# Kernel optimization log

Hardware: AMD Instinct MI355X
Metric: run time of the kernel (lower is better)

Reference implementation:

```python
import jax, jax.numpy as jnp
import numpy as np

B, CIN, COUT = 4, 512, 64
T, H, W = 16, 32, 32


def conv1x1(x, w, b=None):
    # 1x1x1 Conv3d == per-voxel linear: w (out, in), x (b, in, t, h, w)
    y = jnp.einsum('oc,bcthw->bothw', w, x)
    if b is not None:
        y = y + b[None, :, None, None, None]
    return y


def setup_inputs() -> dict:
    key = jax.random.key(0)
    ks = jax.random.split(key, 9)
    def kaiming(k, fan_out_shape):
        out_c, in_c = fan_out_shape
        std = np.sqrt(2.0 / out_c)  # fan_out mode for 1x1x1 kernel
        return jax.random.normal(k, fan_out_shape, dtype=jnp.float32) * std
    c4, c8 = CIN // 4, CIN // 8
    return {
        'x': jax.random.normal(ks[0], (B, CIN, T, H, W), dtype=jnp.float32),
        'w_add1': kaiming(ks[1], (CIN, CIN)), 'b_add1': jnp.zeros((CIN,), jnp.float32),
        'w_add2': kaiming(ks[2], (CIN, CIN)), 'b_add2': jnp.zeros((CIN,), jnp.float32),
        'w_occ1': kaiming(ks[3], (c4, CIN)), 'b_occ1': jnp.zeros((c4,), jnp.float32),
        'w_occ2': kaiming(ks[4], (c8, c4)), 'b_occ2': jnp.zeros((c8,), jnp.float32),
        'w_occ3': kaiming(ks[5], (COUT, c8)),  # bias=False
    }


def reference(x, w_add1, b_add1, w_add2, b_add2, w_occ1, b_occ1, w_occ2, b_occ2, w_occ3):
    # feature_map = add_on_layer(x): conv -> relu -> conv
    feat = conv1x1(jax.nn.relu(conv1x1(x, w_add1, b_add1)), w_add2, b_add2)
    # occ_map = abs(occ(x)): conv -> relu -> conv -> relu -> conv(no bias)
    h = jax.nn.relu(conv1x1(x, w_occ1, b_occ1))
    h = jax.nn.relu(conv1x1(h, w_occ2, b_occ2))
    occ = jnp.abs(conv1x1(h, w_occ3))  # (B, COUT, T, H, W)
    # output with pool='avg': mean over spatial of occ[:, :, None] * feat[:, None]
    # == einsum contraction over T*H*W, avoiding the (B,COUT,CIN,T,H,W) intermediate
    S = T * H * W
    out = jnp.einsum('bothw,bcthw->boc', occ, feat) / S  # (B, COUT, CIN)
    return out
```

## Files before the change

kernel.cpp:

```cpp
#include <hip/hip_runtime.h>


#define S_TOT 16384

typedef __attribute__((ext_vector_type(8))) short bf8_t;
typedef __attribute__((ext_vector_type(4))) short s4_t;
typedef __attribute__((ext_vector_type(4))) float f4_t;

#define MFMA __builtin_amdgcn_mfma_f32_16x16x32_bf16

__device__ __forceinline__ short f2bf(float f) {
  union { float f; unsigned u; } v; v.f = f;
  unsigned u = v.u + 0x7FFFu + ((v.u >> 16) & 1u);
  return (short)(u >> 16);
}

__device__ __forceinline__ void glds16(const void* g, void* l) {
  __builtin_amdgcn_global_load_lds(
      (const __attribute__((address_space(1))) void*)g,
      (__attribute__((address_space(3))) void*)l, 16, 0, 0);
}

__device__ __forceinline__ void stage16k(const short* g, short* lds,
                                         int wv, int lane) {
#pragma unroll
  for (int i = 0; i < 4; ++i) {
    const int off = (wv * 4 + i) * 512;
    glds16(g + off + lane * 8, lds + off);
  }
}

__global__ __launch_bounds__(256) void k_convert(
    const float* __restrict__ w1, const float* __restrict__ wo1,
    const float* __restrict__ wo2, const float* __restrict__ wo3,
    short* __restrict__ dst) {
  int i = blockIdx.x * 256 + threadIdx.x;
  if (i < 262144) {
    const int j = i >> 9, k = i & 511;
    const int di = ((j >> 7) * 8 + (k >> 6)) * 8192 + ((k >> 3) & 7) * 1024 +
                   (j & 127) * 8 + (k & 7);
    dst[di] = f2bf(w1[i]);
  } else if (i < 327680) {
    const int e = i - 262144;
    const int c4 = e >> 9, k = e & 511;
    const int di = 262144 + (k >> 6) * 8192 + ((k >> 3) & 7) * 1024 +
                   c4 * 8 + (k & 7);
    dst[di] = f2bf(wo1[e]);
  } else if (i < 335872) {
    dst[i] = f2bf(wo2[i - 327680]);
  } else if (i < 339968) {
    dst[i] = f2bf(wo3[i - 335872]);
  }
}

__global__ __launch_bounds__(256) void k_transpose(
    const float* __restrict__ x, short* __restrict__ xTs) {
  __shared__ float tls[64][65];
  const int sb = blockIdx.x, cb = blockIdx.y, b = blockIdx.z;
  const int t = threadIdx.x;
  {
    const int cr = t >> 2, ss = (t & 3) * 16;
    const float* src = x + ((size_t)b * 512 + cb * 64 + cr) * S_TOT + sb * 64 + ss;
    f4_t v0 = *(const f4_t*)(src);
    f4_t v1 = *(const f4_t*)(src + 4);
    f4_t v2 = *(const f4_t*)(src + 8);
    f4_t v3 = *(const f4_t*)(src + 12);
#pragma unroll
    for (int j = 0; j < 4; ++j) {
      tls[cr][ss + j]      = v0[j];
      tls[cr][ss + 4 + j]  = v1[j];
      tls[cr][ss + 8 + j]  = v2[j];
      tls[cr][ss + 12 + j] = v3[j];
    }
  }
  __syncthreads();
  {
    const int sr = t >> 2, cs = (t & 3) * 16;
    alignas(16) short tmp[16];
#pragma unroll
    for (int j = 0; j < 16; ++j) tmp[j] = f2bf(tls[cs + j][sr]);
    const int st = sb >> 1, s_in = (sb & 1) * 64 + sr, k8 = cs >> 3;
    short* base = xTs + (((size_t)(b * 128 + st) * 8 + cb) * 8 + k8) * 1024 +
                  s_in * 8;
    *(bf8_t*)base          = *(const bf8_t*)&tmp[0];
    *(bf8_t*)(base + 1024) = *(const bf8_t*)&tmp[8];
  }
}

__global__ __launch_bounds__(256) void k_occ(
    const short* __restrict__ xTs, const short* __restrict__ wo1,
    const short* __restrict__ wo2, const short* __restrict__ wo3,
    const float* __restrict__ bo1, const float* __restrict__ bo2,
    short* __restrict__ occP, float* __restrict__ sumocc) {
  __shared__ short smem[32768];
  short* const buf0 = smem;
  short* const buf1 = smem + 16384;
  short* const h1s = buf0;
  short* const h2s = buf1;
  const int tile = blockIdx.x, b = blockIdx.y;
  const int t = threadIdx.x, lane = t & 63, wv = t >> 6;
  const int q = lane >> 4, li = lane & 15;
  const int mh = (wv & 1) * 64, nh = (wv >> 1) * 64;
  const short* xTb = xTs + (size_t)(b * 128 + tile) * 65536;
  const f4_t fz = {0.f, 0.f, 0.f, 0.f};

  f4_t acc[4][4];
#pragma unroll
  for (int i = 0; i < 4; ++i)
#pragma unroll
    for (int j = 0; j < 4; ++j) acc[i][j] = fz;

  stage16k(xTb, buf1, wv, lane);
  stage16k(wo1, buf1 + 8192, wv, lane);
  int cur = 1;
  for (int i = 0; i < 8; ++i) {
    __syncthreads();
    if (i < 7) {
      short* nb_ = cur ? buf0 : buf1;
      stage16k(xTb + (i + 1) * 8192, nb_, wv, lane);
      stage16k(wo1 + (i + 1) * 8192, nb_ + 8192, wv, lane);
    }
    const short* xs = cur ? buf1 : buf0;
    const short* wsp = xs + 8192;
#pragma unroll
    for (int kk = 0; kk < 2; ++kk) {
      const int pl = (4 * kk + q) * 128;
      bf8_t a[4], bb[4];
#pragma unroll
      for (int ma = 0; ma < 4; ++ma)
        a[ma] = *(const bf8_t*)&wsp[(pl + mh + 16 * ma + li) * 8];
#pragma unroll
      for (int nb = 0; nb < 4; ++nb)
        bb[nb] = *(const bf8_t*)&xs[(pl + nh + 16 * nb + li) * 8];
#pragma unroll
      for (int ma = 0; ma < 4; ++ma)
#pragma unroll
        for (int nb = 0; nb < 4; ++nb)
          acc[ma][nb] = MFMA(a[ma], bb[nb], acc[ma][nb], 0, 0, 0);
    }
    cur ^= 1;
  }
  __syncthreads();
#pragma unroll
  for (int ma = 0; ma < 4; ++ma) {
    const int c40 = mh + 16 * ma + 4 * q;
    f4_t bv = *(const f4_t*)(bo1 + c40);
#pragma unroll
    for (int nb = 0; nb < 4; ++nb) {
      const int sl = nh + 16 * nb + li;
      s4_t p;
#pragma unroll
      for (int r = 0; r < 4; ++r) p[r] = f2bf(fmaxf(acc[ma][nb][r] + bv[r], 0.0f));
      *(s4_t*)&h1s[((c40 >> 3) * 128 + sl) * 8 + (c40 & 7)] = p;
    }
  }
  __syncthreads();
  f4_t a2[4][2];
#pragma unroll
  for (int i = 0; i < 4; ++i) { a2[i][0] = fz; a2[i][1] = fz; }
#pragma unroll
  for (int kk = 0; kk < 4; ++kk) {
    const int pl = (4 * kk + q) * 128;
    bf8_t a[4], bb[2];
#pragma unroll
    for (int ma = 0; ma < 4; ++ma)
      a[ma] = *(const bf8_t*)(wo2 + (size_t)(16 * ma + li) * 128 + kk * 32 + q * 8);
#pragma unroll
    for (int nb = 0; nb < 2; ++nb)
      bb[nb] = *(const bf8_t*)&h1s[(pl + 32 * wv + 16 * nb + li) * 8];
#pragma unroll
    for (int ma = 0; ma < 4; ++ma)
#pragma unroll
      for (int nb = 0; nb < 2; ++nb)
        a2[ma][nb] = MFMA(a[ma], bb[nb], a2[ma][nb], 0, 0, 0);
  }
#pragma unroll
  for (int ma = 0; ma < 4; ++ma) {
    const int c80 = 16 * ma + 4 * q;
    f4_t bv = *(const f4_t*)(bo2 + c80);
#pragma unroll
    for (int nb = 0; nb < 2; ++nb) {
      const int sl = 32 * wv + 16 * nb + li;
      s4_t p;
#pragma unroll
      for (int r = 0; r < 4; ++r) p[r] = f2bf(fmaxf(a2[ma][nb][r] + bv[r], 0.0f));
      *(s4_t*)&h2s[((c80 >> 3) * 128 + sl) * 8 + (c80 & 7)] = p;
    }
  }
  f4_t a3[4][2];
#pragma unroll
  for (int i = 0; i < 4; ++i) { a3[i][0] = fz; a3[i][1] = fz; }
#pragma unroll
  for (int kk = 0; kk < 2; ++kk) {
    const int pl = (4 * kk + q) * 128;
    bf8_t a[4], bb[2];
#pragma unroll
    for (int ma = 0; ma < 4; ++ma)
      a[ma] = *(const bf8_t*)(wo3 + (size_t)(16 * ma + li) * 64 + kk * 32 + q * 8);
#pragma unroll
    for (int nb = 0; nb < 2; ++nb)
      bb[nb] = *(const bf8_t*)&h2s[(pl + 32 * wv + 16 * nb + li) * 8];
#pragma unroll
    for (int ma = 0; ma < 4; ++ma)
#pragma unroll
      for (int nb = 0; nb < 2; ++nb)
        a3[ma][nb] = MFMA(a[ma], bb[nb], a3[ma][nb], 0, 0, 0);
  }
  short* ot = occP + (size_t)(b * 128 + tile) * 8192;
#pragma unroll
  for (int ma = 0; ma < 4; ++ma)
#pragma unroll
    for (int nb = 0; nb < 2; ++nb) {
      const int o = 16 * ma + 4 * q;
      const int sl = 32 * wv + 16 * nb + li;
#pragma unroll
      for (int r = 0; r < 4; ++r)
        ot[(sl >> 3) * 512 + (o + r) * 8 + (sl & 7)] = f2bf(fabsf(a3[ma][nb][r]));
    }
#pragma unroll
  for (int ma = 0; ma < 4; ++ma)
#pragma unroll
    for (int r = 0; r < 4; ++r) {
      float v = fabsf(a3[ma][0][r]) + fabsf(a3[ma][1][r]);
#pragma unroll
      for (int m = 1; m < 16; m <<= 1) v += __shfl_xor(v, m, 64);
      if (li == 0) atomicAdd(&sumocc[b * 64 + 16 * ma + 4 * q + r], v);
    }
}

__global__ __launch_bounds__(256) void k_feat(
    const short* __restrict__ xTs, const short* __restrict__ w1s,
    const float* __restrict__ b1, const short* __restrict__ occP,
    float* __restrict__ M) {
  __shared__ short smem[32768];
  short* const buf0 = smem;
  short* const buf1 = smem + 16384;
  short* const r1s = buf0;
  const int sg = blockIdx.x, cb = blockIdx.y, b = blockIdx.z;
  const int t = threadIdx.x, lane = t & 63, wv = t >> 6;
  const int q = lane >> 4, li = lane & 15;
  const int mh = (wv & 1) * 64, nh = (wv >> 1) * 64;
  const short* w1b = w1s + (size_t)cb * 65536;
  const f4_t fz = {0.f, 0.f, 0.f, 0.f};

  float biasv[4];
#pragma unroll
  for (int nb = 0; nb < 4; ++nb) biasv[nb] = b1[cb * 128 + nh + 16 * nb + li];

  f4_t macc[4][2];
#pragma unroll
  for (int i = 0; i < 4; ++i) { macc[i][0] = fz; macc[i][1] = fz; }

  {
    const short* xT0 = xTs + (size_t)(b * 128 + sg * 4) * 65536;
    stage16k(xT0, buf1, wv, lane);
    stage16k(w1b, buf1 + 8192, wv, lane);
  }

  for (int tt = 0; tt < 4; ++tt) {
    const int st = sg * 4 + tt;
    const short* xTb = xTs + (size_t)(b * 128 + st) * 65536;
    f4_t acc[4][4];
#pragma unroll
    for (int i = 0; i < 4; ++i)
#pragma unroll
      for (int j = 0; j < 4; ++j) acc[i][j] = fz;

    int cur = 1;
    for (int i = 0; i < 8; ++i) {
      __syncthreads();
      if (i < 7) {
        short* nb_ = cur ? buf0 : buf1;
        stage16k(xTb + (i + 1) * 8192, nb_, wv, lane);
        stage16k(w1b + (i + 1) * 8192, nb_ + 8192, wv, lane);
      }
      const short* xs = cur ? buf1 : buf0;
      const short* wsp = xs + 8192;
#pragma unroll
      for (int kk = 0; kk < 2; ++kk) {
        const int pl = (4 * kk + q) * 128;
        bf8_t a[4], bb[4];
#pragma unroll
        for (int ma = 0; ma < 4; ++ma)
          a[ma] = *(const bf8_t*)&xs[(pl + mh + 16 * ma + li) * 8];
#pragma unroll
        for (int nb = 0; nb < 4; ++nb)
          bb[nb] = *(const bf8_t*)&wsp[(pl + nh + 16 * nb + li) * 8];
#pragma unroll
        for (int ma = 0; ma < 4; ++ma)
#pragma unroll
          for (int nb = 0; nb < 4; ++nb)
            acc[ma][nb] = MFMA(a[ma], bb[nb], acc[ma][nb], 0, 0, 0);
      }
      cur ^= 1;
    }
    __syncthreads();
#pragma unroll
    for (int ma = 0; ma < 4; ++ma) {
      const int sl0 = mh + 16 * ma + 4 * q;
#pragma unroll
      for (int nb = 0; nb < 4; ++nb) {
        const int jl = nh + 16 * nb + li;
        s4_t p;
#pragma unroll
        for (int r = 0; r < 4; ++r)
          p[r] = f2bf(fmaxf(acc[ma][nb][r] + biasv[nb], 0.0f));
        *(s4_t*)&r1s[((sl0 >> 3) * 128 + jl) * 8 + (sl0 & 7)] = p;
      }
    }
    __syncthreads();
    if (tt < 3) {
      stage16k(xTb + 65536, buf1, wv, lane);
      stage16k(w1b, buf1 + 8192, wv, lane);
    }
    const short* ot = occP + (size_t)(b * 128 + st) * 8192;
    bf8_t af[4][4];
#pragma unroll
    for (int kc = 0; kc < 4; ++kc)
#pragma unroll
      for (int ma = 0; ma < 4; ++ma)
        af[ma][kc] = *(const bf8_t*)(ot + ((kc * 4 + q) * 64 + 16 * ma + li) * 8);
#pragma unroll
    for (int kc = 0; kc < 4; ++kc) {
      const int pl = (4 * kc + q) * 128;
      bf8_t bb[2];
#pragma unroll
      for (int nb = 0; nb < 2; ++nb)
        bb[nb] = *(const bf8_t*)&r1s[(pl + 32 * wv + 16 * nb + li) * 8];
#pragma unroll
      for (int ma = 0; ma < 4; ++ma)
#pragma unroll
        for (int nb = 0; nb < 2; ++nb)
          macc[ma][nb] = MFMA(af[ma][kc], bb[nb], macc[ma][nb], 0, 0, 0);
    }
  }
#pragma unroll
  for (int ma = 0; ma < 4; ++ma)
#pragma unroll
    for (int nb = 0; nb < 2; ++nb) {
      const int jg = cb * 128 + 32 * wv + 16 * nb + li;
#pragma unroll
      for (int r = 0; r < 4; ++r) {
        const int o = 16 * ma + 4 * q + r;
        atomicAdd(&M[((size_t)b * 64 + o) * 512 + jg], macc[ma][nb][r]);
      }
    }
}

__global__ __launch_bounds__(256) void k_out(
    const float* __restrict__ M, const float* __restrict__ sumocc,
    const float* __restrict__ w2, const float* __restrict__ b2,
    float* __restrict__ out) {
  const int cg = blockIdx.x, og = blockIdx.y, b = blockIdx.z;
  const int t = threadIdx.x;
  const int o = og * 16 + (t >> 4);
  const int c = cg * 16 + (t & 15);
  const float* mr = M + ((size_t)b * 64 + o) * 512;
  const float* wr = w2 + (size_t)c * 512;
  float a = 0.0f;
  for (int j = 0; j < 512; j += 4) {
    f4_t mv = *(const f4_t*)(mr + j);
    f4_t wv = *(const f4_t*)(wr + j);
    a += mv[0] * wv[0] + mv[1] * wv[1] + mv[2] * wv[2] + mv[3] * wv[3];
  }
  out[((size_t)b * 64 + o) * 512 + c] =
      (a + sumocc[b * 64 + o] * b2[c]) * (1.0f / 16384.0f);
}

extern "C" void kernel_launch(void* const* d_in, const int* in_sizes, int n_in,
                              void* d_out, int out_size, void* d_ws, size_t ws_size,
                              hipStream_t stream) {
  (void)in_sizes; (void)n_in; (void)out_size; (void)ws_size;
  const float* x      = (const float*)d_in[0];
  const float* w_add1 = (const float*)d_in[1];
  const float* b_add1 = (const float*)d_in[2];
  const float* w_add2 = (const float*)d_in[3];
  const float* b_add2 = (const float*)d_in[4];
  const float* w_occ1 = (const float*)d_in[5];
  const float* b_occ1 = (const float*)d_in[6];
  const float* w_occ2 = (const float*)d_in[7];
  const float* b_occ2 = (const float*)d_in[8];
  const float* w_occ3 = (const float*)d_in[9];

  char* ws = (char*)d_ws;
  short* xTs     = (short*)(ws);
  short* wb      = (short*)(ws + 67108864);
  short* occP    = (short*)(ws + 67788800);
  float* M       = (float*)(ws + 76177408);
  float* sumocc  = (float*)(ws + 76701696);

  hipMemsetAsync(M, 0, 524288 + 1024, stream);
  k_convert<<<dim3(1328), dim3(256), 0, stream>>>(w_add1, w_occ1, w_occ2, w_occ3, wb);
  k_transpose<<<dim3(256, 8, 4), dim3(256), 0, stream>>>(x, xTs);

  const short* w1sp = wb;
  const short* wbo1 = wb + 262144;
  const short* wbo2 = wb + 327680;
  const short* wbo3 = wb + 335872;
  k_occ<<<dim3(128, 4), dim3(256), 0, stream>>>(xTs, wbo1, wbo2, wbo3,
                                                b_occ1, b_occ2, occP, sumocc);
  k_feat<<<dim3(32, 4, 4), dim3(256), 0, stream>>>(xTs, w1sp, b_add1, occP, M);
  k_out<<<dim3(32, 4, 4), dim3(256), 0, stream>>>(M, sumocc, w_add2, b_add2,
                                                  (float*)d_out);
}
```

Before: 408.0 us.

## Fuse occupancy MLP into feature kernel, keeping occ tile in LDS

Merges k_occ into k_feat. Each feature block now computes the occupancy branch for its own spatial tile from the x tile already staged in LDS, reading w_occ1 fragments directly from global memory. The result goes to LDS instead of a global occP buffer. This removes one kernel launch and the occP write and reread, but each of the four channel blocks recomputes the occupancy MLP, which quadruples that work. It also raises LDS use and register pressure (second 4x4 accumulator, launch_bounds 256,2).

After: 460.8 us. +12.9%, slower.

```diff
diff --git a/kernel.cpp b/kernel.cpp
--- a/kernel.cpp
+++ b/kernel.cpp
@@ -87,155 +87,20 @@
   }
 }
 
-__global__ __launch_bounds__(256) void k_occ(
-    const short* __restrict__ xTs, const short* __restrict__ wo1,
-    const short* __restrict__ wo2, const short* __restrict__ wo3,
-    const float* __restrict__ bo1, const float* __restrict__ bo2,
-    short* __restrict__ occP, float* __restrict__ sumocc) {
-  __shared__ short smem[32768];
+__global__ __launch_bounds__(256, 2) void k_fused(
+    const short* __restrict__ xTs, const short* __restrict__ w1s,
+    const float* __restrict__ b1,
+    const short* __restrict__ wo1, const short* __restrict__ wo2,
+    const short* __restrict__ wo3, const float* __restrict__ bo1,
+    const float* __restrict__ bo2,
+    float* __restrict__ M, float* __restrict__ sumocc) {
+  __shared__ short smem[40960];
   short* const buf0 = smem;
   short* const buf1 = smem + 16384;
+  short* const occS = smem + 32768;
   short* const h1s = buf0;
   short* const h2s = buf1;
-  const int tile = blockIdx.x, b = blockIdx.y;
-  const int t = threadIdx.x, lane = t & 63, wv = t >> 6;
-  const int q = lane >> 4, li = lane & 15;
-  const int mh = (wv & 1) * 64, nh = (wv >> 1) * 64;
-  const short* xTb = xTs + (size_t)(b * 128 + tile) * 65536;
-  const f4_t fz = {0.f, 0.f, 0.f, 0.f};
-
-  f4_t acc[4][4];
-#pragma unroll
-  for (int i = 0; i < 4; ++i)
-#pragma unroll
-    for (int j = 0; j < 4; ++j) acc[i][j] = fz;
-
-  stage16k(xTb, buf1, wv, lane);
-  stage16k(wo1, buf1 + 8192, wv, lane);
-  int cur = 1;
-  for (int i = 0; i < 8; ++i) {
-    __syncthreads();
-    if (i < 7) {
-      short* nb_ = cur ? buf0 : buf1;
-      stage16k(xTb + (i + 1) * 8192, nb_, wv, lane);
-      stage16k(wo1 + (i + 1) * 8192, nb_ + 8192, wv, lane);
-    }
-    const short* xs = cur ? buf1 : buf0;
-    const short* wsp = xs + 8192;
-#pragma unroll
-    for (int kk = 0; kk < 2; ++kk) {
-      const int pl = (4 * kk + q) * 128;
-      bf8_t a[4], bb[4];
-#pragma unroll
-      for (int ma = 0; ma < 4; ++ma)
-        a[ma] = *(const bf8_t*)&wsp[(pl + mh + 16 * ma + li) * 8];
-#pragma unroll
-      for (int nb = 0; nb < 4; ++nb)
-        bb[nb] = *(const bf8_t*)&xs[(pl + nh + 16 * nb + li) * 8];
-#pragma unroll
-      for (int ma = 0; ma < 4; ++ma)
-#pragma unroll
-        for (int nb = 0; nb < 4; ++nb)
-          acc[ma][nb] = MFMA(a[ma], bb[nb], acc[ma][nb], 0, 0, 0);
-    }
-    cur ^= 1;
-  }
-  __syncthreads();
-#pragma unroll
-  for (int ma = 0; ma < 4; ++ma) {
-    const int c40 = mh + 16 * ma + 4 * q;
-    f4_t bv = *(const f4_t*)(bo1 + c40);
-#pragma unroll
-    for (int nb = 0; nb < 4; ++nb) {
-      const int sl = nh + 16 * nb + li;
-      s4_t p;
-#pragma unroll
-      for (int r = 0; r < 4; ++r) p[r] = f2bf(fmaxf(acc[ma][nb][r] + bv[r], 0.0f));
-      *(s4_t*)&h1s[((c40 >> 3) * 128 + sl) * 8 + (c40 & 7)] = p;
-    }
-  }
-  __syncthreads();
-  f4_t a2[4][2];
-#pragma unroll
-  for (int i = 0; i < 4; ++i) { a2[i][0] = fz; a2[i][1] = fz; }
-#pragma unroll
-  for (int kk = 0; kk < 4; ++kk) {
-    const int pl = (4 * kk + q) * 128;
-    bf8_t a[4], bb[2];
-#pragma unroll
-    for (int ma = 0; ma < 4; ++ma)
-      a[ma] = *(const bf8_t*)(wo2 + (size_t)(16 * ma + li) * 128 + kk * 32 + q * 8);
-#pragma unroll
-    for (int nb = 0; nb < 2; ++nb)
-      bb[nb] = *(const bf8_t*)&h1s[(pl + 32 * wv + 16 * nb + li) * 8];
-#pragma unroll
-    for (int ma = 0; ma < 4; ++ma)
-#pragma unroll
-      for (int nb = 0; nb < 2; ++nb)
-        a2[ma][nb] = MFMA(a[ma], bb[nb], a2[ma][nb], 0, 0, 0);
-  }
-#pragma unroll
-  for (int ma = 0; ma < 4; ++ma) {
-    const int c80 = 16 * ma + 4 * q;
-    f4_t bv = *(const f4_t*)(bo2 + c80);
-#pragma unroll
-    for (int nb = 0; nb < 2; ++nb) {
-      const int sl = 32 * wv + 16 * nb + li;
-      s4_t p;
-#pragma unroll
-      for (int r = 0; r < 4; ++r) p[r] = f2bf(fmaxf(a2[ma][nb][r] + bv[r], 0.0f));
-      *(s4_t*)&h2s[((c80 >> 3) * 128 + sl) * 8 + (c80 & 7)] = p;
-    }
-  }
-  f4_t a3[4][2];
-#pragma unroll
-  for (int i = 0; i < 4; ++i) { a3[i][0] = fz; a3[i][1] = fz; }
-#pragma unroll
-  for (int kk = 0; kk < 2; ++kk) {
-    const int pl = (4 * kk + q) * 128;
-    bf8_t a[4], bb[2];
-#pragma unroll
-    for (int ma = 0; ma < 4; ++ma)
-      a[ma] = *(const bf8_t*)(wo3 + (size_t)(16 * ma + li) * 64 + kk * 32 + q * 8);
-#pragma unroll
-    for (int nb = 0; nb < 2; ++nb)
-      bb[nb] = *(const bf8_t*)&h2s[(pl + 32 * wv + 16 * nb + li) * 8];
-#pragma unroll
-    for (int ma = 0; ma < 4; ++ma)
-#pragma unroll
-      for (int nb = 0; nb < 2; ++nb)
-        a3[ma][nb] = MFMA(a[ma], bb[nb], a3[ma][nb], 0, 0, 0);
-  }
-  short* ot = occP + (size_t)(b * 128 + tile) * 8192;
-#pragma unroll
-  for (int ma = 0; ma < 4; ++ma)
-#pragma unroll
-    for (int nb = 0; nb < 2; ++nb) {
-      const int o = 16 * ma + 4 * q;
-      const int sl = 32 * wv + 16 * nb + li;
-#pragma unroll
-      for (int r = 0; r < 4; ++r)
-        ot[(sl >> 3) * 512 + (o + r) * 8 + (sl & 7)] = f2bf(fabsf(a3[ma][nb][r]));
-    }
-#pragma unroll
-  for (int ma = 0; ma < 4; ++ma)
-#pragma unroll
-    for (int r = 0; r < 4; ++r) {
-      float v = fabsf(a3[ma][0][r]) + fabsf(a3[ma][1][r]);
-#pragma unroll
-      for (int m = 1; m < 16; m <<= 1) v += __shfl_xor(v, m, 64);
-      if (li == 0) atomicAdd(&sumocc[b * 64 + 16 * ma + 4 * q + r], v);
-    }
-}
-
-__global__ __launch_bounds__(256) void k_feat(
-    const short* __restrict__ xTs, const short* __restrict__ w1s,
-    const float* __restrict__ b1, const short* __restrict__ occP,
-    float* __restrict__ M) {
-  __shared__ short smem[32768];
-  short* const buf0 = smem;
-  short* const buf1 = smem + 16384;
-  short* const r1s = buf0;
+  short* const r1s = buf1;
   const int sg = blockIdx.x, cb = blockIdx.y, b = blockIdx.z;
   const int t = threadIdx.x, lane = t & 63, wv = t >> 6;
   const int q = lane >> 4, li = lane & 15;
@@ -253,48 +118,147 @@
 
   {
     const short* xT0 = xTs + (size_t)(b * 128 + sg * 4) * 65536;
-    stage16k(xT0, buf1, wv, lane);
-    stage16k(w1b, buf1 + 8192, wv, lane);
+    stage16k(xT0, buf0, wv, lane);
+    stage16k(w1b, buf0 + 8192, wv, lane);
   }
 
   for (int tt = 0; tt < 4; ++tt) {
     const int st = sg * 4 + tt;
     const short* xTb = xTs + (size_t)(b * 128 + st) * 65536;
     f4_t acc[4][4];
+    f4_t hcc[4][4];
 #pragma unroll
     for (int i = 0; i < 4; ++i)
 #pragma unroll
-      for (int j = 0; j < 4; ++j) acc[i][j] = fz;
-
-    int cur = 1;
+      for (int j = 0; j < 4; ++j) { acc[i][j] = fz; hcc[i][j] = fz; }
+
     for (int i = 0; i < 8; ++i) {
       __syncthreads();
       if (i < 7) {
-        short* nb_ = cur ? buf0 : buf1;
+        short* nb_ = ((i + 1) & 1) ? buf1 : buf0;
         stage16k(xTb + (i + 1) * 8192, nb_, wv, lane);
         stage16k(w1b + (i + 1) * 8192, nb_ + 8192, wv, lane);
       }
-      const short* xs = cur ? buf1 : buf0;
+      const short* xs = (i & 1) ? buf1 : buf0;
       const short* wsp = xs + 8192;
+      const short* og = wo1 + i * 8192;
 #pragma unroll
       for (int kk = 0; kk < 2; ++kk) {
         const int pl = (4 * kk + q) * 128;
-        bf8_t a[4], bb[4];
+        bf8_t xa[4], xb[4], wf[4], of[4];
 #pragma unroll
         for (int ma = 0; ma < 4; ++ma)
-          a[ma] = *(const bf8_t*)&xs[(pl + mh + 16 * ma + li) * 8];
+          xa[ma] = *(const bf8_t*)&xs[(pl + mh + 16 * ma + li) * 8];
 #pragma unroll
         for (int nb = 0; nb < 4; ++nb)
-          bb[nb] = *(const bf8_t*)&wsp[(pl + nh + 16 * nb + li) * 8];
+          xb[nb] = *(const bf8_t*)&xs[(pl + nh + 16 * nb + li) * 8];
+#pragma unroll
+        for (int nb = 0; nb < 4; ++nb)
+          wf[nb] = *(const bf8_t*)&wsp[(pl + nh + 16 * nb + li) * 8];
 #pragma unroll
         for (int ma = 0; ma < 4; ++ma)
-#pragma unroll
-          for (int nb = 0; nb < 4; ++nb)
-            acc[ma][nb] = MFMA(a[ma], bb[nb], acc[ma][nb], 0, 0, 0);
-      }
-      cur ^= 1;
+          of[ma] = *(const bf8_t*)&og[(pl + mh + 16 * ma + li) * 8];
+#pragma unroll
+        for (int ma = 0; ma < 4; ++ma)
+#pragma unroll
+          for (int nb = 0; nb < 4; ++nb) {
+            acc[ma][nb] = MFMA(xa[ma], wf[nb], acc[ma][nb], 0, 0, 0);
+            hcc[ma][nb] = MFMA(of[ma], xb[nb], hcc[ma][nb], 0, 0, 0);
+          }
+      }
     }
     __syncthreads();
+#pragma unroll
+    for (int ma = 0; ma < 4; ++ma) {
+      const int c40 = mh + 16 * ma + 4 * q;
+      f4_t bv = *(const f4_t*)(bo1 + c40);
+#pragma unroll
+      for (int nb = 0; nb < 4; ++nb) {
+        const int sl = nh + 16 * nb + li;
+        s4_t p;
+#pragma unroll
+        for (int r = 0; r < 4; ++r) p[r] = f2bf(fmaxf(hcc[ma][nb][r] + bv[r], 0.0f));
+        *(s4_t*)&h1s[((c40 >> 3) * 128 + sl) * 8 + (c40 & 7)] = p;
+      }
+    }
+    __syncthreads();
+    f4_t a2[4][2];
+#pragma unroll
+    for (int i = 0; i < 4; ++i) { a2[i][0] = fz; a2[i][1] = fz; }
+#pragma unroll
+    for (int kk = 0; kk < 4; ++kk) {
+      const int pl = (4 * kk + q) * 128;
+      bf8_t a[4], bb[2];
+#pragma unroll
+      for (int ma = 0; ma < 4; ++ma)
+        a[ma] = *(const bf8_t*)(wo2 + (size_t)(16 * ma + li) * 128 + kk * 32 + q * 8);
+#pragma unroll
+      for (int nb = 0; nb < 2; ++nb)
+        bb[nb] = *(const bf8_t*)&h1s[(pl + 32 * wv + 16 * nb + li) * 8];
+#pragma unroll
+      for (int ma = 0; ma < 4; ++ma)
+#pragma unroll
+        for (int nb = 0; nb < 2; ++nb)
+          a2[ma][nb] = MFMA(a[ma], bb[nb], a2[ma][nb], 0, 0, 0);
+    }
+#pragma unroll
+    for (int ma = 0; ma < 4; ++ma) {
+      const int c80 = 16 * ma + 4 * q;
+      f4_t bv = *(const f4_t*)(bo2 + c80);
+#pragma unroll
+      for (int nb = 0; nb < 2; ++nb) {
+        const int sl = 32 * wv + 16 * nb + li;
+        s4_t p;
+#pragma unroll
+        for (int r = 0; r < 4; ++r) p[r] = f2bf(fmaxf(a2[ma][nb][r] + bv[r], 0.0f));
+        *(s4_t*)&h2s[((c80 >> 3) * 128 + sl) * 8 + (c80 & 7)] = p;
+      }
+    }
+    f4_t a3[4][2];
+#pragma unroll
+    for (int i = 0; i < 4; ++i) { a3[i][0] = fz; a3[i][1] = fz; }
+#pragma unroll
+    for (int kk = 0; kk < 2; ++kk) {
+      const int pl = (4 * kk + q) * 128;
+      bf8_t a[4], bb[2];
+#pragma unroll
+      for (int ma = 0; ma < 4; ++ma)
+        a[ma] = *(const bf8_t*)(wo3 + (size_t)(16 * ma + li) * 64 + kk * 32 + q * 8);
+#pragma unroll
+      for (int nb = 0; nb < 2; ++nb)
+        bb[nb] = *(const bf8_t*)&h2s[(pl + 32 * wv + 16 * nb + li) * 8];
+#pragma unroll
+      for (int ma = 0; ma < 4; ++ma)
+#pragma unroll
+        for (int nb = 0; nb < 2; ++nb)
+          a3[ma][nb] = MFMA(a[ma], bb[nb], a3[ma][nb], 0, 0, 0);
+    }
+#pragma unroll
+    for (int ma = 0; ma < 4; ++ma)
+#pragma unroll
+      for (int nb = 0; nb < 2; ++nb) {
+        const int o = 16 * ma + 4 * q;
+        const int sl = 32 * wv + 16 * nb + li;
+#pragma unroll
+        for (int r = 0; r < 4; ++r)
+          occS[(sl >> 3) * 512 + (o + r) * 8 + (sl & 7)] = f2bf(fabsf(a3[ma][nb][r]));
+      }
+    if (cb == 0) {
+#pragma unroll
+      for (int ma = 0; ma < 4; ++ma)
+#pragma unroll
+        for (int r = 0; r < 4; ++r) {
+          float v = fabsf(a3[ma][0][r]) + fabsf(a3[ma][1][r]);
+#pragma unroll
+          for (int m = 1; m < 16; m <<= 1) v += __shfl_xor(v, m, 64);
+          if (li == 0) atomicAdd(&sumocc[b * 64 + 16 * ma + 4 * q + r], v);
+        }
+    }
+    __syncthreads();
+    if (tt < 3) {
+      stage16k(xTb + 65536, buf0, wv, lane);
+      stage16k(w1b, buf0 + 8192, wv, lane);
+    }
 #pragma unroll
     for (int ma = 0; ma < 4; ++ma) {
       const int sl0 = mh + 16 * ma + 4 * q;
@@ -309,17 +273,12 @@
       }
     }
     __syncthreads();
-    if (tt < 3) {
-      stage16k(xTb + 65536, buf1, wv, lane);
-      stage16k(w1b, buf1 + 8192, wv, lane);
-    }
-    const short* ot = occP + (size_t)(b * 128 + st) * 8192;
     bf8_t af[4][4];
 #pragma unroll
     for (int kc = 0; kc < 4; ++kc)
 #pragma unroll
       for (int ma = 0; ma < 4; ++ma)
-        af[ma][kc] = *(const bf8_t*)(ot + ((kc * 4 + q) * 64 + 16 * ma + li) * 8);
+        af[ma][kc] = *(const bf8_t*)&occS[((kc * 4 + q) * 64 + 16 * ma + li) * 8];
 #pragma unroll
     for (int kc = 0; kc < 4; ++kc) {
       const int pl = (4 * kc + q) * 128;
@@ -385,7 +344,6 @@
   char* ws = (char*)d_ws;
   short* xTs     = (short*)(ws);
   short* wb      = (short*)(ws + 67108864);
-  short* occP    = (short*)(ws + 67788800);
   float* M       = (float*)(ws + 76177408);
   float* sumocc  = (float*)(ws + 76701696);
 
@@ -397,9 +355,8 @@
   const short* wbo1 = wb + 262144;
   const short* wbo2 = wb + 327680;
   const short* wbo3 = wb + 335872;
-  k_occ<<<dim3(128, 4), dim3(256), 0, stream>>>(xTs, wbo1, wbo2, wbo3,
-                                                b_occ1, b_occ2, occP, sumocc);
-  k_feat<<<dim3(32, 4, 4), dim3(256), 0, stream>>>(xTs, w1sp, b_add1, occP, M);
+  k_fused<<<dim3(32, 4, 4), dim3(256), 0, stream>>>(
+      xTs, w1sp, b_add1, wbo1, wbo2, wbo3, b_occ1, b_occ2, M, sumocc);
   k_out<<<dim3(32, 4, 4), dim3(256), 0, stream>>>(M, sumocc, w_add2, b_add2,
                                                   (float*)d_out);
 }
```

## Load MFMA operands directly from global memory instead of LDS double-buffering

Applied to the files above, without the earlier changes.

Drops the global_load_lds double-buffered staging in k_occ and k_feat and reads the bf16 operand fragments straight from global memory into registers, fully unrolling the K loop. This removes the per-step __syncthreads barriers and halves LDS use, and together with launch_bounds(256,3) aims for more resident blocks per CU. In exchange, data reuse now relies on L1/L2 caches rather than shared memory, so global traffic and load latency may go up, and the occupancy hint may cause register spills.

Result: slower. 547.1 us (+34.1%).

```diff
diff --git a/kernel.cpp b/kernel.cpp
--- a/kernel.cpp
+++ b/kernel.cpp
@@ -13,21 +13,6 @@
   union { float f; unsigned u; } v; v.f = f;
   unsigned u = v.u + 0x7FFFu + ((v.u >> 16) & 1u);
   return (short)(u >> 16);
-}
-
-__device__ __forceinline__ void glds16(const void* g, void* l) {
-  __builtin_amdgcn_global_load_lds(
-      (const __attribute__((address_space(1))) void*)g,
-      (__attribute__((address_space(3))) void*)l, 16, 0, 0);
-}
-
-__device__ __forceinline__ void stage16k(const short* g, short* lds,
-                                         int wv, int lane) {
-#pragma unroll
-  for (int i = 0; i < 4; ++i) {
-    const int off = (wv * 4 + i) * 512;
-    glds16(g + off + lane * 8, lds + off);
-  }
 }
 
 __global__ __launch_bounds__(256) void k_convert(
@@ -87,16 +72,14 @@
   }
 }
 
-__global__ __launch_bounds__(256) void k_occ(
+__global__ __launch_bounds__(256, 3) void k_occ(
     const short* __restrict__ xTs, const short* __restrict__ wo1,
     const short* __restrict__ wo2, const short* __restrict__ wo3,
     const float* __restrict__ bo1, const float* __restrict__ bo2,
     short* __restrict__ occP, float* __restrict__ sumocc) {
-  __shared__ short smem[32768];
-  short* const buf0 = smem;
-  short* const buf1 = smem + 16384;
-  short* const h1s = buf0;
-  short* const h2s = buf1;
+  __shared__ short smem[24576];
+  short* const h1s = smem;
+  short* const h2s = smem + 16384;
   const int tile = blockIdx.x, b = blockIdx.y;
   const int t = threadIdx.x, lane = t & 63, wv = t >> 6;
   const int q = lane >> 4, li = lane & 15;
@@ -104,31 +87,23 @@
   const short* xTb = xTs + (size_t)(b * 128 + tile) * 65536;
   const f4_t fz = {0.f, 0.f, 0.f, 0.f};
 
-  f4_t acc[4][4];
+  f4_t hcc[4][4];
 #pragma unroll
   for (int i = 0; i < 4; ++i)
 #pragma unroll
-    for (int j = 0; j < 4; ++j) acc[i][j] = fz;
-
-  stage16k(xTb, buf1, wv, lane);
-  stage16k(wo1, buf1 + 8192, wv, lane);
-  int cur = 1;
+    for (int j = 0; j < 4; ++j) hcc[i][j] = fz;
+
+#pragma unroll
   for (int i = 0; i < 8; ++i) {
-    __syncthreads();
-    if (i < 7) {
-      short* nb_ = cur ? buf0 : buf1;
-      stage16k(xTb + (i + 1) * 8192, nb_, wv, lane);
-      stage16k(wo1 + (i + 1) * 8192, nb_ + 8192, wv, lane);
-    }
-    const short* xs = cur ? buf1 : buf0;
-    const short* wsp = xs + 8192;
+    const short* xs = xTb + i * 8192;
+    const short* og = wo1 + i * 8192;
 #pragma unroll
     for (int kk = 0; kk < 2; ++kk) {
       const int pl = (4 * kk + q) * 128;
       bf8_t a[4], bb[4];
 #pragma unroll
       for (int ma = 0; ma < 4; ++ma)
-        a[ma] = *(const bf8_t*)&wsp[(pl + mh + 16 * ma + li) * 8];
+        a[ma] = *(const bf8_t*)&og[(pl + mh + 16 * ma + li) * 8];
 #pragma unroll
       for (int nb = 0; nb < 4; ++nb)
         bb[nb] = *(const bf8_t*)&xs[(pl + nh + 16 * nb + li) * 8];
@@ -136,11 +111,9 @@
       for (int ma = 0; ma < 4; ++ma)
 #pragma unroll
         for (int nb = 0; nb < 4; ++nb)
-          acc[ma][nb] = MFMA(a[ma], bb[nb], acc[ma][nb], 0, 0, 0);
-    }
-    cur ^= 1;
-  }
-  __syncthreads();
+          hcc[ma][nb] = MFMA(a[ma], bb[nb], hcc[ma][nb], 0, 0, 0);
+    }
+  }
 #pragma unroll
   for (int ma = 0; ma < 4; ++ma) {
     const int c40 = mh + 16 * ma + 4 * q;
@@ -150,7 +123,7 @@
       const int sl = nh + 16 * nb + li;
       s4_t p;
 #pragma unroll
-      for (int r = 0; r < 4; ++r) p[r] = f2bf(fmaxf(acc[ma][nb][r] + bv[r], 0.0f));
+      for (int r = 0; r < 4; ++r) p[r] = f2bf(fmaxf(hcc[ma][nb][r] + bv[r], 0.0f));
       *(s4_t*)&h1s[((c40 >> 3) * 128 + sl) * 8 + (c40 & 7)] = p;
     }
   }
@@ -228,14 +201,11 @@
     }
 }
 
-__global__ __launch_bounds__(256) void k_feat(
+__global__ __launch_bounds__(256, 3) void k_feat(
     const short* __restrict__ xTs, const short* __restrict__ w1s,
     const float* __restrict__ b1, const short* __restrict__ occP,
     float* __restrict__ M) {
-  __shared__ short smem[32768];
-  short* const buf0 = smem;
-  short* const buf1 = smem + 16384;
-  short* const r1s = buf0;
+  __shared__ short r1s[16384];
   const int sg = blockIdx.x, cb = blockIdx.y, b = blockIdx.z;
   const int t = threadIdx.x, lane = t & 63, wv = t >> 6;
   const int q = lane >> 4, li = lane & 15;
@@ -251,12 +221,6 @@
 #pragma unroll
   for (int i = 0; i < 4; ++i) { macc[i][0] = fz; macc[i][1] = fz; }
 
-  {
-    const short* xT0 = xTs + (size_t)(b * 128 + sg * 4) * 65536;
-    stage16k(xT0, buf1, wv, lane);
-    stage16k(w1b, buf1 + 8192, wv, lane);
-  }
-
   for (int tt = 0; tt < 4; ++tt) {
     const int st = sg * 4 + tt;
     const short* xTb = xTs + (size_t)(b * 128 + st) * 65536;
@@ -266,16 +230,10 @@
 #pragma unroll
       for (int j = 0; j < 4; ++j) acc[i][j] = fz;
 
-    int cur = 1;
+#pragma unroll
     for (int i = 0; i < 8; ++i) {
-      __syncthreads();
-      if (i < 7) {
-        short* nb_ = cur ? buf0 : buf1;
-        stage16k(xTb + (i + 1) * 8192, nb_, wv, lane);
-        stage16k(w1b + (i + 1) * 8192, nb_ + 8192, wv, lane);
-      }
-      const short* xs = cur ? buf1 : buf0;
-      const short* wsp = xs + 8192;
+      const short* xs = xTb + i * 8192;
+      const short* wsp = w1b + i * 8192;
 #pragma unroll
       for (int kk = 0; kk < 2; ++kk) {
         const int pl = (4 * kk + q) * 128;
@@ -292,7 +250,6 @@
           for (int nb = 0; nb < 4; ++nb)
             acc[ma][nb] = MFMA(a[ma], bb[nb], acc[ma][nb], 0, 0, 0);
       }
-      cur ^= 1;
     }
     __syncthreads();
 #pragma unroll
@@ -309,10 +266,6 @@
       }
     }
     __syncthreads();
-    if (tt < 3) {
-      stage16k(xTb + 65536, buf1, wv, lane);
-      stage16k(w1b, buf1 + 8192, wv, lane);
-    }
     const short* ot = occP + (size_t)(b * 128 + st) * 8192;
     bf8_t af[4][4];
 #pragma unroll
```

## Fuse weight conversion into transpose, use explicit vmcnt waits in GEMM pipelines

Applied to the files above, without the earlier changes.

Folds the weight bf16 conversion kernel into the transpose kernel, run by the blocks with cb==0 and b==0, which removes one launch. In the double-buffered k_occ and k_feat loops it replaces __syncthreads with raw s_barrier plus explicit s_waitcnt vmcnt(8)/vmcnt(0), so the next tile's global-to-LDS loads stay in flight while the current tile is consumed. It also moves the occP fragment loads ahead of the next stage prefetch so the vmcnt ordering stays correct. The risks are load imbalance from the 256 blocks that also convert weights, and correctness that depends on the hand-placed wait counts.

Measured after the change: 396.9 us. -2.7%, faster.

```diff
diff --git a/kernel.cpp b/kernel.cpp
--- a/kernel.cpp
+++ b/kernel.cpp
@@ -8,6 +8,12 @@
 typedef __attribute__((ext_vector_type(4))) float f4_t;
 
 #define MFMA __builtin_amdgcn_mfma_f32_16x16x32_bf16
+
+#define BAR_FENCE() do { __builtin_amdgcn_s_barrier(); \
+                         asm volatile("" ::: "memory"); } while (0)
+#define WAIT_VM8()  asm volatile("s_waitcnt vmcnt(8)" ::: "memory")
+#define WAIT_VM0()  asm volatile("s_waitcnt vmcnt(0)" ::: "memory")
+#define WAIT_LGKM0() asm volatile("s_waitcnt lgkmcnt(0)" ::: "memory")
 
 __device__ __forceinline__ short f2bf(float f) {
   union { float f; unsigned u; } v; v.f = f;
@@ -30,34 +36,34 @@
   }
 }
 
-__global__ __launch_bounds__(256) void k_convert(
+__global__ __launch_bounds__(256) void k_transpose(
+    const float* __restrict__ x, short* __restrict__ xTs,
     const float* __restrict__ w1, const float* __restrict__ wo1,
     const float* __restrict__ wo2, const float* __restrict__ wo3,
-    short* __restrict__ dst) {
-  int i = blockIdx.x * 256 + threadIdx.x;
-  if (i < 262144) {
-    const int j = i >> 9, k = i & 511;
-    const int di = ((j >> 7) * 8 + (k >> 6)) * 8192 + ((k >> 3) & 7) * 1024 +
-                   (j & 127) * 8 + (k & 7);
-    dst[di] = f2bf(w1[i]);
-  } else if (i < 327680) {
-    const int e = i - 262144;
-    const int c4 = e >> 9, k = e & 511;
-    const int di = 262144 + (k >> 6) * 8192 + ((k >> 3) & 7) * 1024 +
-                   c4 * 8 + (k & 7);
-    dst[di] = f2bf(wo1[e]);
-  } else if (i < 335872) {
-    dst[i] = f2bf(wo2[i - 327680]);
-  } else if (i < 339968) {
-    dst[i] = f2bf(wo3[i - 335872]);
-  }
-}
-
-__global__ __launch_bounds__(256) void k_transpose(
-    const float* __restrict__ x, short* __restrict__ xTs) {
+    short* __restrict__ wb) {
   __shared__ float tls[64][65];
   const int sb = blockIdx.x, cb = blockIdx.y, b = blockIdx.z;
   const int t = threadIdx.x;
+  if (cb == 0 && b == 0) {
+    for (int i = sb * 256 + t; i < 339968; i += 65536) {
+      if (i < 262144) {
+        const int j = i >> 9, k = i & 511;
+        const int di = ((j >> 7) * 8 + (k >> 6)) * 8192 +
+                       ((k >> 3) & 7) * 1024 + (j & 127) * 8 + (k & 7);
+        wb[di] = f2bf(w1[i]);
+      } else if (i < 327680) {
+        const int e = i - 262144;
+        const int c4 = e >> 9, k = e & 511;
+        const int di = 262144 + (k >> 6) * 8192 + ((k >> 3) & 7) * 1024 +
+                       c4 * 8 + (k & 7);
+        wb[di] = f2bf(wo1[e]);
+      } else if (i < 335872) {
+        wb[i] = f2bf(wo2[i - 327680]);
+      } else {
+        wb[i] = f2bf(wo3[i - 335872]);
+      }
+    }
+  }
   {
     const int cr = t >> 2, ss = (t & 3) * 16;
     const float* src = x + ((size_t)b * 512 + cb * 64 + cr) * S_TOT + sb * 64 + ss;
@@ -104,23 +110,26 @@
   const short* xTb = xTs + (size_t)(b * 128 + tile) * 65536;
   const f4_t fz = {0.f, 0.f, 0.f, 0.f};
 
-  f4_t acc[4][4];
+  f4_t hcc[4][4];
 #pragma unroll
   for (int i = 0; i < 4; ++i)
 #pragma unroll
-    for (int j = 0; j < 4; ++j) acc[i][j] = fz;
+    for (int j = 0; j < 4; ++j) hcc[i][j] = fz;
 
   stage16k(xTb, buf1, wv, lane);
   stage16k(wo1, buf1 + 8192, wv, lane);
-  int cur = 1;
   for (int i = 0; i < 8; ++i) {
-    __syncthreads();
+    BAR_FENCE();
     if (i < 7) {
-      short* nb_ = cur ? buf0 : buf1;
+      short* nb_ = (i & 1) ? buf1 : buf0;
       stage16k(xTb + (i + 1) * 8192, nb_, wv, lane);
       stage16k(wo1 + (i + 1) * 8192, nb_ + 8192, wv, lane);
-    }
-    const short* xs = cur ? buf1 : buf0;
+      WAIT_VM8();
+    } else {
+      WAIT_VM0();
+    }
+    BAR_FENCE();
+    const short* xs = (i & 1) ? buf0 : buf1;
     const short* wsp = xs + 8192;
 #pragma unroll
     for (int kk = 0; kk < 2; ++kk) {
@@ -136,11 +145,11 @@
       for (int ma = 0; ma < 4; ++ma)
 #pragma unroll
         for (int nb = 0; nb < 4; ++nb)
-          acc[ma][nb] = MFMA(a[ma], bb[nb], acc[ma][nb], 0, 0, 0);
-    }
-    cur ^= 1;
-  }
-  __syncthreads();
+          hcc[ma][nb] = MFMA(a[ma], bb[nb], hcc[ma][nb], 0, 0, 0);
+    }
+  }
+  WAIT_LGKM0();
+  BAR_FENCE();
 #pragma unroll
   for (int ma = 0; ma < 4; ++ma) {
     const int c40 = mh + 16 * ma + 4 * q;
@@ -150,7 +159,7 @@
       const int sl = nh + 16 * nb + li;
       s4_t p;
 #pragma unroll
-      for (int r = 0; r < 4; ++r) p[r] = f2bf(fmaxf(acc[ma][nb][r] + bv[r], 0.0f));
+      for (int r = 0; r < 4; ++r) p[r] = f2bf(fmaxf(hcc[ma][nb][r] + bv[r], 0.0f));
       *(s4_t*)&h1s[((c40 >> 3) * 128 + sl) * 8 + (c40 & 7)] = p;
     }
   }
@@ -266,15 +275,18 @@
 #pragma unroll
       for (int j = 0; j < 4; ++j) acc[i][j] = fz;
 
-    int cur = 1;
     for (int i = 0; i < 8; ++i) {
-      __syncthreads();
+      BAR_FENCE();
       if (i < 7) {
-        short* nb_ = cur ? buf0 : buf1;
+        short* nb_ = (i & 1) ? buf1 : buf0;
         stage16k(xTb + (i + 1) * 8192, nb_, wv, lane);
         stage16k(w1b + (i + 1) * 8192, nb_ + 8192, wv, lane);
+        WAIT_VM8();
+      } else {
+        WAIT_VM0();
       }
-      const short* xs = cur ? buf1 : buf0;
+      BAR_FENCE();
+      const short* xs = (i & 1) ? buf0 : buf1;
       const short* wsp = xs + 8192;
 #pragma unroll
       for (int kk = 0; kk < 2; ++kk) {
@@ -292,9 +304,9 @@
           for (int nb = 0; nb < 4; ++nb)
             acc[ma][nb] = MFMA(a[ma], bb[nb], acc[ma][nb], 0, 0, 0);
       }
-      cur ^= 1;
-    }
-    __syncthreads();
+    }
+    WAIT_LGKM0();
+    BAR_FENCE();
 #pragma unroll
     for (int ma = 0; ma < 4; ++ma) {
       const int sl0 = mh + 16 * ma + 4 * q;
@@ -308,18 +320,19 @@
         *(s4_t*)&r1s[((sl0 >> 3) * 128 + jl) * 8 + (sl0 & 7)] = p;
       }
     }
-    __syncthreads();
+    WAIT_LGKM0();
+    BAR_FENCE();
+    const short* ot = occP + (size_t)(b * 128 + st) * 8192;
+    bf8_t af[4][4];
+#pragma unroll
+    for (int kc = 0; kc < 4; ++kc)
+#pragma unroll
+      for (int ma = 0; ma < 4; ++ma)
+        af[ma][kc] = *(const bf8_t*)(ot + ((kc * 4 + q) * 64 + 16 * ma + li) * 8);
     if (tt < 3) {
       stage16k(xTb + 65536, buf1, wv, lane);
       stage16k(w1b, buf1 + 8192, wv, lane);
     }
-    const short* ot = occP + (size_t)(b * 128 + st) * 8192;
-    bf8_t af[4][4];
-#pragma unroll
-    for (int kc = 0; kc < 4; ++kc)
-#pragma unroll
-      for (int ma = 0; ma < 4; ++ma)
-        af[ma][kc] = *(const bf8_t*)(ot + ((kc * 4 + q) * 64 + 16 * ma + li) * 8);
 #pragma unroll
     for (int kc = 0; kc < 4; ++kc) {
       const int pl = (4 * kc + q) * 128;
@@ -390,8 +403,8 @@
   float* sumocc  = (float*)(ws + 76701696);
 
   hipMemsetAsync(M, 0, 524288 + 1024, stream);
-  k_convert<<<dim3(1328), dim3(256), 0, stream>>>(w_add1, w_occ1, w_occ2, w_occ3, wb);
-  k_transpose<<<dim3(256, 8, 4), dim3(256), 0, stream>>>(x, xTs);
+  k_transpose<<<dim3(256, 8, 4), dim3(256), 0, stream>>>(
+      x, xTs, w_add1, w_occ1, w_occ2, w_occ3, wb);
 
   const short* w1sp = wb;
   const short* wbo1 = wb + 262144;
```
